# Performance work log

Measured on AMD Instinct MI355X. Metric: run time of the kernel, lower is better.

Reference implementation:

```python
import jax, jax.numpy as jnp
import numpy as np

VOCAB = 30000
EMB = 100
HID = 300
SEQ = 200
BATCH = 4096


def setup_inputs() -> dict:
    key = jax.random.key(0)
    ks = jax.random.split(key, 10)
    s_ih = 1.0 / np.sqrt(HID)
    inp = {
        "x": jax.random.randint(ks[0], (SEQ, BATCH), 0, VOCAB, dtype=jnp.int64) if jax.config.jax_enable_x64 else jax.random.randint(ks[0], (SEQ, BATCH), 0, VOCAB, dtype=jnp.int32),
        "emb": jax.random.normal(ks[1], (VOCAB, EMB), dtype=jnp.float32),
        "w_ih": jax.random.uniform(ks[2], (HID, EMB), jnp.float32, -s_ih, s_ih),
        "w_hh": jax.random.uniform(ks[3], (HID, HID), jnp.float32, -s_ih, s_ih),
        "b_ih": jax.random.uniform(ks[4], (HID,), jnp.float32, -s_ih, s_ih),
        "b_hh": jax.random.uniform(ks[5], (HID,), jnp.float32, -s_ih, s_ih),
        "fc1_w": jax.random.uniform(ks[6], (256, HID), jnp.float32, -1/np.sqrt(HID), 1/np.sqrt(HID)),
        "fc1_b": jax.random.uniform(ks[7], (256,), jnp.float32, -1/np.sqrt(HID), 1/np.sqrt(HID)),
        "fc2_w": jax.random.uniform(ks[8], (3, 256), jnp.float32, -1/np.sqrt(256), 1/np.sqrt(256)),
        "fc2_b": jax.random.uniform(ks[9], (3,), jnp.float32, -1/np.sqrt(256), 1/np.sqrt(256)),
    }
    return inp


def reference(x, emb, w_ih, w_hh, b_ih, b_hh, fc1_w, fc1_b, fc2_w, fc2_b):
    # Embedding lookup: [SEQ, BATCH] -> [SEQ, BATCH, EMB]
    xe = emb[x]
    # Precompute input projections for all timesteps (same math, more efficient)
    xp = jnp.einsum('sbe,he->sbh', xe, w_ih) + b_ih + b_hh  # [SEQ, BATCH, HID]
    h0 = jnp.zeros((x.shape[1], HID), dtype=emb.dtype)

    def step(h, xt):
        h = jnp.tanh(xt + h @ w_hh.T)
        return h, None

    ht, _ = jax.lax.scan(step, h0, xp)
    h1 = jax.nn.relu(ht @ fc1_w.T + fc1_b)
    out = h1 @ fc2_w.T + fc2_b
    return out
```

## Files before the change

### kernel.cpp

```cpp
#include <hip/hip_runtime.h>


#define SEQ    200
#define BATCHN 4096
#define EMBD   100
#define HIDN   300

#define KCH  19
#define KCE  7
#define XE0  304
#define SROW 436
#define ROWS 16

typedef _Float16 half4 __attribute__((ext_vector_type(4)));
typedef float    f32x4 __attribute__((ext_vector_type(4)));

static __device__ __forceinline__ half4 h4cvt(f32x4 v) {
  half4 h; h[0]=(_Float16)v[0]; h[1]=(_Float16)v[1];
  h[2]=(_Float16)v[2]; h[3]=(_Float16)v[3];
  return h;
}
static __device__ __forceinline__ half4 h4zero() {
  half4 h; h[0]=(_Float16)0.f; h[1]=(_Float16)0.f;
  h[2]=(_Float16)0.f; h[3]=(_Float16)0.f;
  return h;
}
static __device__ __forceinline__ float tanh_fast(float x) {
  float e = __builtin_amdgcn_exp2f(x * 2.8853900817779268f);
  float r = __builtin_amdgcn_rcpf(e + 1.0f);
  return __builtin_fmaf(-2.0f, r, 1.0f);
}

#define MFMA16(A,B,C) __builtin_amdgcn_mfma_f32_16x16x16f16((A),(B),(C),0,0,0)

#define STEP_BODY(NT_) do {                                                   \
    _Pragma("unroll")                                                         \
    for (int c = 0; c < KCH; c++) {                                           \
      const half4 a = *(const half4*)(a_base + c * 16);                       \
      acc[0] = MFMA16(a, whh[c][0], acc[0]);                                  \
      acc[1] = MFMA16(a, whh[c][1], acc[1]);                                  \
      if (NT_ == 3) acc[2] = MFMA16(a, whh[c][2], acc[2]);                    \
    }                                                                         \
    _Pragma("unroll")                                                         \
    for (int c = 0; c < KCE; c++) {                                           \
      const half4 a = *(const half4*)(a_base + XE0 + c * 16);                 \
      acc[0] = MFMA16(a, wih[c][0], acc[0]);                                  \
      acc[1] = MFMA16(a, wih[c][1], acc[1]);                                  \
      if (NT_ == 3) acc[2] = MFMA16(a, wih[c][2], acc[2]);                    \
    }                                                                         \
  } while (0)

__global__ __launch_bounds__(512, 2)
void rnn_fused(const int* __restrict__ x, const float* __restrict__ emb,
               const float* __restrict__ w_ih, const float* __restrict__ w_hh,
               const float* __restrict__ b_ih, const float* __restrict__ b_hh,
               const float* __restrict__ fc1w, const float* __restrict__ fc1b,
               const float* __restrict__ fc2w, const float* __restrict__ fc2b,
               float* __restrict__ out)
{
  __shared__ __align__(16) _Float16 s_lds[ROWS][SROW];
  __shared__ __align__(16) float    h1f[ROWS][257];
  __shared__ int x_lds[SEQ][16];

  const int tid  = (int)threadIdx.x;
  const int lane = tid & 63;
  const int wv   = tid >> 6;
  const int r    = lane & 15;
  const int g    = lane >> 4;
  const int base = (int)blockIdx.x * ROWS;

  const int t0    = (wv < 3) ? wv * 3 : 9 + (wv - 3) * 2;
  const int ntile = (wv < 3) ? 3 : 2;

  for (int i = tid; i < SEQ * 16; i += 512)
    x_lds[i >> 4][i & 15] = x[(i >> 4) * BATCHN + base + (i & 15)];
  for (int i = tid; i < ROWS * SROW; i += 512)
    (&s_lds[0][0])[i] = (_Float16)0.f;

  half4 whh[KCH][3];
  half4 wih[KCE][3];
  float bias[3];
  #pragma unroll
  for (int tt = 0; tt < 3; tt++) {
    const int n = (t0 + tt) * 16 + r;
    const bool nv = (tt < ntile) && (n < HIDN);
    bias[tt] = nv ? (b_ih[n] + b_hh[n]) : 0.f;
    #pragma unroll
    for (int c = 0; c < KCH; c++) {
      const int k = c * 16 + 4 * g;
      whh[c][tt] = (nv && k < HIDN)
          ? h4cvt(*(const f32x4*)(w_hh + (long)n * HIDN + k)) : h4zero();
    }
    #pragma unroll
    for (int c = 0; c < KCE; c++) {
      const int k = c * 16 + 4 * g;
      wih[c][tt] = (nv && k < EMBD)
          ? h4cvt(*(const f32x4*)(w_ih + (long)n * EMBD + k)) : h4zero();
    }
  }

  const int gc0 = (wv == 6) ? 0 : 4;
  const int gcn = (wv == 6) ? 4 : 3;

  __syncthreads();

  if (wv >= 6) {
    const int idx = x_lds[0][r];
    const float* erow = emb + (long)idx * EMBD;
    #pragma unroll
    for (int j = 0; j < 4; j++) {
      const int c = gc0 + j, k = c * 16 + 4 * g;
      if (j < gcn && k < EMBD)
        *(half4*)&s_lds[r][XE0 + c * 16 + 4 * g] = h4cvt(*(const f32x4*)(erow + k));
    }
  }
  __syncthreads();

  const _Float16* a_base = &s_lds[r][4 * g];

  #pragma unroll 1
  for (int t = 0; t < SEQ; t++) {
    f32x4 xg[4];
    if (wv >= 6) {
      const int tn = (t + 1 < SEQ) ? t + 1 : t;
      const int idx = x_lds[tn][r];
      const float* erow = emb + (long)idx * EMBD;
      #pragma unroll
      for (int j = 0; j < 4; j++) {
        const int c = gc0 + j, k = c * 16 + 4 * g;
        if (j < gcn && k < EMBD) xg[j] = *(const f32x4*)(erow + k);
      }
    }

    f32x4 acc[3];
    #pragma unroll
    for (int tt = 0; tt < 3; tt++) {
      f32x4 v = {bias[tt], bias[tt], bias[tt], bias[tt]};
      acc[tt] = v;
    }

    if (ntile == 3) { STEP_BODY(3); } else { STEP_BODY(2); }

    __syncthreads();

    if (wv >= 6) {
      #pragma unroll
      for (int j = 0; j < 4; j++) {
        const int c = gc0 + j, k = c * 16 + 4 * g;
        if (j < gcn && k < EMBD)
          *(half4*)&s_lds[r][XE0 + c * 16 + 4 * g] = h4cvt(xg[j]);
      }
    }
    #pragma unroll
    for (int tt = 0; tt < 3; tt++) {
      if (tt < ntile) {
        const int n = (t0 + tt) * 16 + r;
        if (n < HIDN) {
          #pragma unroll
          for (int j = 0; j < 4; j++)
            s_lds[4 * g + j][n] = (_Float16)tanh_fast(acc[tt][j]);
        }
      }
    }
    __syncthreads();
  }

  {
    f32x4 acc1[2];
    const int f0 = wv * 2;
    #pragma unroll
    for (int ft = 0; ft < 2; ft++) {
      const float bb = fc1b[(f0 + ft) * 16 + r];
      f32x4 v = {bb, bb, bb, bb};
      acc1[ft] = v;
    }
    #pragma unroll
    for (int c = 0; c < KCH; c++) {
      const half4 a = *(const half4*)(a_base + c * 16);
      const int k = c * 16 + 4 * g;
      #pragma unroll
      for (int ft = 0; ft < 2; ft++) {
        const int n = (f0 + ft) * 16 + r;
        const half4 b = (k < HIDN)
            ? h4cvt(*(const f32x4*)(fc1w + (long)n * HIDN + k)) : h4zero();
        acc1[ft] = MFMA16(a, b, acc1[ft]);
      }
    }
    #pragma unroll
    for (int ft = 0; ft < 2; ft++) {
      const int n = (f0 + ft) * 16 + r;
      #pragma unroll
      for (int j = 0; j < 4; j++) {
        const float v = acc1[ft][j];
        h1f[4 * g + j][n] = v > 0.f ? v : 0.f;
      }
    }
  }
  __syncthreads();

  if (wv == 0 && lane < 48) {
    const int m = lane / 3;
    const int n = lane - 3 * m;
    float s = fc2b[n];
    for (int k = 0; k < 256; k++)
      s = __builtin_fmaf(h1f[m][k], fc2w[n * 256 + k], s);
    out[(base + m) * 3 + n] = s;
  }
}

extern "C" void kernel_launch(void* const* d_in, const int* in_sizes, int n_in,
                              void* d_out, int out_size, void* d_ws, size_t ws_size,
                              hipStream_t stream) {
  (void)in_sizes; (void)n_in; (void)d_ws; (void)ws_size; (void)out_size;
  const int*   x   = (const int*)d_in[0];
  const float* emb = (const float*)d_in[1];
  const float* wih = (const float*)d_in[2];
  const float* whh = (const float*)d_in[3];
  const float* bih = (const float*)d_in[4];
  const float* bhh = (const float*)d_in[5];
  const float* f1w = (const float*)d_in[6];
  const float* f1b = (const float*)d_in[7];
  const float* f2w = (const float*)d_in[8];
  const float* f2b = (const float*)d_in[9];
  rnn_fused<<<BATCHN / ROWS, 512, 0, stream>>>(
      x, emb, wih, whh, bih, bhh, f1w, f1b, f2w, f2b, (float*)d_out);
}
```

Before: 404.9 us.

## Use 16x16x32 MFMA and double-buffered LDS state to drop a barrier per step

Switches the recurrent and input GEMMs from 16x16x16 to 16x16x32 f16 MFMA, halving the number of MFMA and LDS-read instructions per timestep. The hidden-state and embedding LDS buffer is double-buffered by timestep parity, so writes for step t+1 go to the other half and one of the two __syncthreads per step can be removed. This doubles the LDS row size and changes the K-padding layout, which may raise LDS use and bank conflicts.

Result: faster. 337.6 us (-16.6%).

```diff
diff --git a/kernel.cpp b/kernel.cpp
--- a/kernel.cpp
+++ b/kernel.cpp
@@ -6,47 +6,53 @@
 #define EMBD   100
 #define HIDN   300
 
-#define KCH  19
-#define KCE  7
-#define XE0  304
-#define SROW 436
-#define ROWS 16
-
-typedef _Float16 half4 __attribute__((ext_vector_type(4)));
+#define KCH   10
+#define KCE   4
+#define XE0   320
+#define BSPAN 448
+#define SROW  904
+#define ROWS  16
+
+typedef _Float16 half8 __attribute__((ext_vector_type(8)));
 typedef float    f32x4 __attribute__((ext_vector_type(4)));
 
-static __device__ __forceinline__ half4 h4cvt(f32x4 v) {
-  half4 h; h[0]=(_Float16)v[0]; h[1]=(_Float16)v[1];
-  h[2]=(_Float16)v[2]; h[3]=(_Float16)v[3];
+static __device__ __forceinline__ f32x4 f4z() { f32x4 z = {0.f, 0.f, 0.f, 0.f}; return z; }
+
+static __device__ __forceinline__ half8 h8cvt(f32x4 a, f32x4 b) {
+  half8 h;
+  h[0]=(_Float16)a[0]; h[1]=(_Float16)a[1]; h[2]=(_Float16)a[2]; h[3]=(_Float16)a[3];
+  h[4]=(_Float16)b[0]; h[5]=(_Float16)b[1]; h[6]=(_Float16)b[2]; h[7]=(_Float16)b[3];
   return h;
 }
-static __device__ __forceinline__ half4 h4zero() {
-  half4 h; h[0]=(_Float16)0.f; h[1]=(_Float16)0.f;
-  h[2]=(_Float16)0.f; h[3]=(_Float16)0.f;
-  return h;
-}
+
+static __device__ __forceinline__ half8 loadw(const float* row, int k0, int kmax, bool nv) {
+  f32x4 a = (nv && (k0 + 3 < kmax)) ? *(const f32x4*)(row + k0)     : f4z();
+  f32x4 b = (nv && (k0 + 7 < kmax)) ? *(const f32x4*)(row + k0 + 4) : f4z();
+  return h8cvt(a, b);
+}
+
 static __device__ __forceinline__ float tanh_fast(float x) {
   float e = __builtin_amdgcn_exp2f(x * 2.8853900817779268f);
   float r = __builtin_amdgcn_rcpf(e + 1.0f);
   return __builtin_fmaf(-2.0f, r, 1.0f);
 }
 
-#define MFMA16(A,B,C) __builtin_amdgcn_mfma_f32_16x16x16f16((A),(B),(C),0,0,0)
+#define MFMA32(A,B,C) __builtin_amdgcn_mfma_f32_16x16x32_f16((A),(B),(C),0,0,0)
 
 #define STEP_BODY(NT_) do {                                                   \
     _Pragma("unroll")                                                         \
     for (int c = 0; c < KCH; c++) {                                           \
-      const half4 a = *(const half4*)(a_base + c * 16);                       \
-      acc[0] = MFMA16(a, whh[c][0], acc[0]);                                  \
-      acc[1] = MFMA16(a, whh[c][1], acc[1]);                                  \
-      if (NT_ == 3) acc[2] = MFMA16(a, whh[c][2], acc[2]);                    \
+      const half8 a = *(const half8*)(ab + c * 32);                           \
+      acc[0] = MFMA32(a, whh[c][0], acc[0]);                                  \
+      acc[1] = MFMA32(a, whh[c][1], acc[1]);                                  \
+      if (NT_ == 3) acc[2] = MFMA32(a, whh[c][2], acc[2]);                    \
     }                                                                         \
     _Pragma("unroll")                                                         \
     for (int c = 0; c < KCE; c++) {                                           \
-      const half4 a = *(const half4*)(a_base + XE0 + c * 16);                 \
-      acc[0] = MFMA16(a, wih[c][0], acc[0]);                                  \
-      acc[1] = MFMA16(a, wih[c][1], acc[1]);                                  \
-      if (NT_ == 3) acc[2] = MFMA16(a, wih[c][2], acc[2]);                    \
+      const half8 a = *(const half8*)(ab + XE0 + c * 32);                     \
+      acc[0] = MFMA32(a, wih[c][0], acc[0]);                                  \
+      acc[1] = MFMA32(a, wih[c][1], acc[1]);                                  \
+      if (NT_ == 3) acc[2] = MFMA32(a, wih[c][2], acc[2]);                    \
     }                                                                         \
   } while (0)
 
@@ -77,8 +83,8 @@
   for (int i = tid; i < ROWS * SROW; i += 512)
     (&s_lds[0][0])[i] = (_Float16)0.f;
 
-  half4 whh[KCH][3];
-  half4 wih[KCE][3];
+  half8 whh[KCH][3];
+  half8 wih[KCE][3];
   float bias[3];
   #pragma unroll
   for (int tt = 0; tt < 3; tt++) {
@@ -86,21 +92,14 @@
     const bool nv = (tt < ntile) && (n < HIDN);
     bias[tt] = nv ? (b_ih[n] + b_hh[n]) : 0.f;
     #pragma unroll
-    for (int c = 0; c < KCH; c++) {
-      const int k = c * 16 + 4 * g;
-      whh[c][tt] = (nv && k < HIDN)
-          ? h4cvt(*(const f32x4*)(w_hh + (long)n * HIDN + k)) : h4zero();
-    }
-    #pragma unroll
-    for (int c = 0; c < KCE; c++) {
-      const int k = c * 16 + 4 * g;
-      wih[c][tt] = (nv && k < EMBD)
-          ? h4cvt(*(const f32x4*)(w_ih + (long)n * EMBD + k)) : h4zero();
-    }
-  }
-
-  const int gc0 = (wv == 6) ? 0 : 4;
-  const int gcn = (wv == 6) ? 4 : 3;
+    for (int c = 0; c < KCH; c++)
+      whh[c][tt] = loadw(w_hh + (long)n * HIDN, c * 32 + 8 * g, HIDN, nv);
+    #pragma unroll
+    for (int c = 0; c < KCE; c++)
+      wih[c][tt] = loadw(w_ih + (long)n * EMBD, c * 32 + 8 * g, EMBD, nv);
+  }
+
+  const int gc0 = (wv - 6) * 2;
 
   __syncthreads();
 
@@ -108,27 +107,32 @@
     const int idx = x_lds[0][r];
     const float* erow = emb + (long)idx * EMBD;
     #pragma unroll
-    for (int j = 0; j < 4; j++) {
-      const int c = gc0 + j, k = c * 16 + 4 * g;
-      if (j < gcn && k < EMBD)
-        *(half4*)&s_lds[r][XE0 + c * 16 + 4 * g] = h4cvt(*(const f32x4*)(erow + k));
+    for (int j = 0; j < 2; j++) {
+      const int k0 = (gc0 + j) * 32 + 8 * g;
+      f32x4 a = (k0 + 3 < EMBD) ? *(const f32x4*)(erow + k0)     : f4z();
+      f32x4 b = (k0 + 7 < EMBD) ? *(const f32x4*)(erow + k0 + 4) : f4z();
+      *(half8*)&s_lds[r][XE0 + k0] = h8cvt(a, b);
     }
   }
   __syncthreads();
 
-  const _Float16* a_base = &s_lds[r][4 * g];
-
-  #pragma unroll 1
+  const _Float16* a_base = &s_lds[r][8 * g];
+
+  #pragma unroll 2
   for (int t = 0; t < SEQ; t++) {
-    f32x4 xg[4];
+    const _Float16* ab = a_base + (t & 1) * BSPAN;
+    const int nbuf = ((t + 1) & 1) * BSPAN;
+
+    f32x4 xg[2][2];
     if (wv >= 6) {
       const int tn = (t + 1 < SEQ) ? t + 1 : t;
       const int idx = x_lds[tn][r];
       const float* erow = emb + (long)idx * EMBD;
       #pragma unroll
-      for (int j = 0; j < 4; j++) {
-        const int c = gc0 + j, k = c * 16 + 4 * g;
-        if (j < gcn && k < EMBD) xg[j] = *(const f32x4*)(erow + k);
+      for (int j = 0; j < 2; j++) {
+        const int k0 = (gc0 + j) * 32 + 8 * g;
+        xg[j][0] = (k0 + 3 < EMBD) ? *(const f32x4*)(erow + k0)     : f4z();
+        xg[j][1] = (k0 + 7 < EMBD) ? *(const f32x4*)(erow + k0 + 4) : f4z();
       }
     }
 
@@ -141,14 +145,11 @@
 
     if (ntile == 3) { STEP_BODY(3); } else { STEP_BODY(2); }
 
-    __syncthreads();
-
     if (wv >= 6) {
       #pragma unroll
-      for (int j = 0; j < 4; j++) {
-        const int c = gc0 + j, k = c * 16 + 4 * g;
-        if (j < gcn && k < EMBD)
-          *(half4*)&s_lds[r][XE0 + c * 16 + 4 * g] = h4cvt(xg[j]);
+      for (int j = 0; j < 2; j++) {
+        const int k0 = (gc0 + j) * 32 + 8 * g;
+        *(half8*)&s_lds[r][nbuf + XE0 + k0] = h8cvt(xg[j][0], xg[j][1]);
       }
     }
     #pragma unroll
@@ -158,7 +159,7 @@
         if (n < HIDN) {
           #pragma unroll
           for (int j = 0; j < 4; j++)
-            s_lds[4 * g + j][n] = (_Float16)tanh_fast(acc[tt][j]);
+            s_lds[4 * g + j][nbuf + n] = (_Float16)tanh_fast(acc[tt][j]);
         }
       }
     }
@@ -166,6 +167,7 @@
   }
 
   {
+    const _Float16* abf = a_base + (SEQ & 1) * BSPAN;
     f32x4 acc1[2];
     const int f0 = wv * 2;
     #pragma unroll
@@ -176,14 +178,12 @@
     }
     #pragma unroll
     for (int c = 0; c < KCH; c++) {
-      const half4 a = *(const half4*)(a_base + c * 16);
-      const int k = c * 16 + 4 * g;
+      const half8 a = *(const half8*)(abf + c * 32);
       #pragma unroll
       for (int ft = 0; ft < 2; ft++) {
         const int n = (f0 + ft) * 16 + r;
-        const half4 b = (k < HIDN)
-            ? h4cvt(*(const f32x4*)(fc1w + (long)n * HIDN + k)) : h4zero();
-        acc1[ft] = MFMA16(a, b, acc1[ft]);
+        const half8 b = loadw(fc1w + (long)n * HIDN, c * 32 + 8 * g, HIDN, true);
+        acc1[ft] = MFMA32(a, b, acc1[ft]);
       }
     }
     #pragma unroll
```
